# Kernel optimization log

Measured on AMD Instinct MI355X. Metric: run time of the kernel, lower is better.

The kernel has to match this reference:

```python
import jax, jax.numpy as jnp
import numpy as np

BQ, BP, L, CIN, H1, H2, COUT = 32, 256, 16, 8192, 256, 32, 8192


def _conv_block(x, w1, b1, w2, b2, w3, b3):
    # x: (B, L, H1) -> Conv1d stack over token dim with residual, as in self.convs
    h = jnp.transpose(x, (0, 2, 1))  # (B, H1, L)
    for w, b in ((w1, b1), (w2, b2), (w3, b3)):
        h = jax.lax.conv_general_dilated(h, w, (1,), [(2, 2)],
                                         dimension_numbers=('NCH', 'OIH', 'NCH'))
        h = jax.nn.relu(h + b[None, :, None])
    return jnp.transpose(h, (0, 2, 1)) + x


def setup_inputs() -> dict:
    key = jax.random.key(0)
    ks = jax.random.split(key, 16)
    query_x = (jax.random.uniform(ks[0], (BQ, L, CIN)) < 0.01).astype(jnp.float32)
    poi_x = (jax.random.uniform(ks[1], (BP, L, CIN)) < 0.01).astype(jnp.float32)
    query_loc = jax.random.uniform(ks[2], (BQ, 2)) * 100.0
    poi_loc = jax.random.uniform(ks[3], (BP, 2)) * 100.0
    enc_w = jax.random.normal(ks[4], (H1, CIN)) * 0.02
    conv_w1 = jax.random.normal(ks[5], (H1, H1, 5)) * 0.02
    conv_w2 = jax.random.normal(ks[6], (H1, H1, 5)) * 0.02
    conv_w3 = jax.random.normal(ks[7], (H1, H1, 5)) * 0.02
    conv_b1 = jnp.zeros((H1,), jnp.float32)
    conv_b2 = jnp.zeros((H1,), jnp.float32)
    conv_b3 = jnp.zeros((H1,), jnp.float32)
    dec_w1 = jax.random.normal(ks[8], (H2, 2 * H1)) * 0.05
    dec_b1 = jnp.zeros((H2,), jnp.float32)
    dec_w2 = jax.random.normal(ks[9], (H2, H2)) * 0.1
    dec_b2 = jnp.zeros((H2,), jnp.float32)
    # torch init fills this with 0; use small randn so the path is non-trivial
    dec_w3 = jax.random.normal(ks[10], (COUT, H2)) * 0.01
    a = jnp.asarray(1.0, jnp.float32)
    b = jnp.asarray(0.0, jnp.float32)
    c = jnp.asarray(1.0, jnp.float32)
    d = jnp.asarray(0.0, jnp.float32)
    return dict(query_x=query_x, query_loc=query_loc, poi_x=poi_x, poi_loc=poi_loc,
                enc_w=enc_w, conv_w1=conv_w1, conv_b1=conv_b1, conv_w2=conv_w2,
                conv_b2=conv_b2, conv_w3=conv_w3, conv_b3=conv_b3,
                dec_w1=dec_w1, dec_b1=dec_b1, dec_w2=dec_w2, dec_b2=dec_b2,
                dec_w3=dec_w3, a=a, b=b, c=c, d=d)


def reference(query_x, query_loc, poi_x, poi_loc, enc_w, conv_w1, conv_b1,
              conv_w2, conv_b2, conv_w3, conv_b3, dec_w1, dec_b1, dec_w2,
              dec_b2, dec_w3, a, b, c, d):
    # --- encode ---
    q_h = _conv_block(query_x @ enc_w.T, conv_w1, conv_b1, conv_w2, conv_b2, conv_w3, conv_b3)
    p_h = _conv_block(poi_x @ enc_w.T, conv_w1, conv_b1, conv_w2, conv_b2, conv_w3, conv_b3)
    q_emb = q_h.mean(axis=1)  # (Bq, H1)
    p_emb = p_h.mean(axis=1)  # (Bp, H1)
    # --- bloom masks ---
    q_bloom = jnp.minimum(query_x.sum(axis=1), 1.0)  # (Bq, 8192)
    p_bloom = jnp.minimum(poi_x.sum(axis=1), 1.0)    # (Bp, 8192)
    interaction = q_bloom[:, None, :] * p_bloom[None, :, :]  # (Bq, Bp, 8192)
    q_bits = q_bloom.sum(axis=-1, keepdims=True)             # (Bq, 1)
    # --- pairwise MLP decode ---
    bq, bp = q_emb.shape[0], p_emb.shape[0]
    all_embed = jnp.concatenate([
        jnp.broadcast_to(q_emb[:, None, :], (bq, bp, q_emb.shape[-1])),
        jnp.broadcast_to(p_emb[None, :, :], (bq, bp, p_emb.shape[-1])),
    ], axis=-1)  # (Bq, Bp, 2*H1)
    h = jax.nn.relu(all_embed)
    h = jax.nn.relu(h @ dec_w1.T + dec_b1)
    h = jax.nn.relu(h @ dec_w2.T + dec_b2)
    w = h @ dec_w3.T  # (Bq, Bp, 8192)
    weights = jnp.where(w >= 0, w, w * 0.125) + 1.0  # LeakyReLU(1/8) + 1
    desc_sim = (interaction * weights).sum(axis=-1) / q_bits  # (Bq, Bp)
    # --- geo-distance fusion ---
    dist = jnp.sqrt(((query_loc[:, None, :] - poi_loc[None, :, :]) ** 2).sum(axis=-1))
    mean = desc_sim.mean(axis=-1, keepdims=True)
    std = jnp.std(desc_sim, axis=-1, keepdims=True, ddof=1)  # torch.std is unbiased
    desc_sim = (desc_sim - mean) / (std + 1e-6)
    dist_sim = -jnp.log(dist + 1.0)
    return (c - jax.nn.sigmoid(a * desc_sim + b)) * (dist_sim - d)
```

## Files before the change

kernel.cpp:

```cpp
#include <hip/hip_runtime.h>

#define NB 288
#define NBQ 32
#define NBP 256
#define LTOK 16
#define CIN 8192
#define H1 256
#define H2 32
#define MASKW 256
#define XROW 264
#define IDXCAP 208

typedef __attribute__((ext_vector_type(8))) short short8;
typedef __attribute__((ext_vector_type(4))) float f32x4;

__device__ __forceinline__ unsigned short f2bf(float f) {
    unsigned u = __float_as_uint(f);
    u += 0x7fffu + ((u >> 16) & 1u);
    return (unsigned short)(u >> 16);
}

__global__ __launch_bounds__(256) void k_transpose_pack(const float* __restrict__ w,
                                                        unsigned* __restrict__ wtp) {
    __shared__ float tile[32][33];
    int k0 = blockIdx.x * 32;
    int h0 = blockIdx.y * 32;
    int tx = threadIdx.x & 31, ty = threadIdx.x >> 5;
#pragma unroll
    for (int i = 0; i < 32; i += 8)
        tile[ty + i][tx] = w[(h0 + ty + i) * CIN + k0 + tx];
    __syncthreads();
    int kl = threadIdx.x >> 3, pw = threadIdx.x & 7;
#pragma unroll
    for (int u = 0; u < 2; ++u) {
        int p = pw + u * 8;
        unsigned lo = f2bf(tile[2 * p][kl]);
        unsigned hi = f2bf(tile[2 * p + 1][kl]);
        wtp[(size_t)(k0 + kl) * 128 + (h0 >> 1) + p] = (hi << 16) | lo;
    }
}

__global__ __launch_bounds__(256) void k_wprep(const float* __restrict__ w1,
                                               const float* __restrict__ w2,
                                               const float* __restrict__ w3,
                                               unsigned short* __restrict__ wtb,
                                               unsigned* __restrict__ wtp) {
    int bx = blockIdx.x;
    if (bx == 0 && threadIdx.x < 128) wtp[(size_t)8192 * 128 + threadIdx.x] = 0;
    int l = bx / 1280;
    int r = bx - l * 1280;
    int o = r / 5;
    int d = r - o * 5;
    int i = threadIdx.x;
    const float* w = (l == 0) ? w1 : (l == 1) ? w2 : w3;
    wtb[(size_t)l * 327680 + (size_t)o * 1280 + d * 256 + i] =
        f2bf(w[(size_t)o * 1280 + i * 5 + d]);
}

__global__ __launch_bounds__(256) void k_w3pack(const float* __restrict__ w3,
                                                unsigned* __restrict__ w3p) {
    int idx = blockIdx.x * 256 + threadIdx.x;
    int k = idx >> 4, pw = idx & 15;
    unsigned lo = f2bf(w3[k * 32 + 2 * pw]);
    unsigned hi = f2bf(w3[k * 32 + 2 * pw + 1]);
    w3p[idx] = (hi << 16) | lo;
}

__global__ __launch_bounds__(256) void k_scan(const float* __restrict__ qx,
                                              const float* __restrict__ px,
                                              int* __restrict__ idxl,
                                              int* __restrict__ cnts,
                                              unsigned* __restrict__ masks) {
    int row = blockIdx.x;
    int b = row >> 4;
    const float* x = (b < NBQ) ? (qx + (size_t)row * CIN)
                               : (px + (size_t)(row - NBQ * LTOK) * CIN);
    __shared__ int cnt;
    int tid = threadIdx.x;
    if (tid == 0) cnt = 0;
    __syncthreads();
    const float4* x4 = (const float4*)x;
    float4 r[8];
#pragma unroll
    for (int j = 0; j < 8; ++j) r[j] = x4[j * 256 + tid];
    int* il = idxl + (size_t)row * IDXCAP;
#pragma unroll
    for (int j = 0; j < 8; ++j) {
        unsigned ox = __float_as_uint(r[j].x) | __float_as_uint(r[j].y) |
                      __float_as_uint(r[j].z) | __float_as_uint(r[j].w);
        if (ox) {
            int base = (j * 256 + tid) * 4;
            float vv[4] = {r[j].x, r[j].y, r[j].z, r[j].w};
#pragma unroll
            for (int c = 0; c < 4; ++c) {
                if (vv[c] != 0.f) {
                    int k = base + c;
                    int p = atomicAdd(&cnt, 1);
                    if (p < 192) il[p] = k;
                    atomicOr(&masks[b * MASKW + (k >> 5)], 1u << (k & 31));
                }
            }
        }
    }
    __syncthreads();
    int n = min(cnt, 192);
    if (tid == 0) cnts[row] = n;
    for (int i = n + tid; i < 200; i += 256) il[i] = 8192;
}

__global__ __launch_bounds__(128) void k_gather(const unsigned* __restrict__ wtp,
                                                const int* __restrict__ idxl,
                                                const int* __restrict__ cnts,
                                                float* __restrict__ encoded,
                                                unsigned* __restrict__ xbufu) {
    int row = blockIdx.x, tid = threadIdx.x;
    int n = cnts[row];
    const int* il = idxl + (size_t)row * IDXCAP;
    float aL = 0.f, aH = 0.f;
    for (int j = 0; j < n; j += 8) {
        int4 ia = *(const int4*)(il + j);
        int4 ib = *(const int4*)(il + j + 4);
        int id[8] = {ia.x, ia.y, ia.z, ia.w, ib.x, ib.y, ib.z, ib.w};
#pragma unroll
        for (int u = 0; u < 8; ++u) {
            unsigned v = wtp[(size_t)id[u] * 128 + tid];
            aL += __uint_as_float(v << 16);
            aH += __uint_as_float(v & 0xffff0000u);
        }
    }
    ((float2*)encoded)[(size_t)row * 128 + tid] = float2{aL, aH};
    unsigned bl = f2bf(aL), bh = f2bf(aH);
    xbufu[(size_t)row * 128 + tid] = (bh << 16) | bl;
}

__global__ __launch_bounds__(256) void k_cgemm(const unsigned short* __restrict__ actIn,
                                               unsigned short* __restrict__ actOut,
                                               float* __restrict__ actOutF,
                                               const unsigned short* __restrict__ wl,
                                               const float* __restrict__ bias,
                                               int last) {
    __shared__ unsigned short Als[2 * 20 * XROW];
    __shared__ unsigned short Bls[32 * XROW];
    int tid = threadIdx.x;
    int m0 = blockIdx.x * 32, n0 = blockIdx.y * 32;

    int* Ai = (int*)Als;
#pragma unroll
    for (int i = tid; i < 20 * XROW; i += 256) Ai[i] = 0;
    __syncthreads();

    int row = tid >> 3, part = tid & 7;
    {
        const short8* src = (const short8*)(actIn + (size_t)(m0 + row) * 256 + part * 32);
        unsigned short* dst = Als + ((row >> 4) * 20 + (row & 15) + 2) * XROW + part * 32;
#pragma unroll
        for (int j = 0; j < 4; ++j) *(short8*)(dst + j * 8) = src[j];
    }
    const unsigned short* bsrc = wl + (size_t)(n0 + row) * 1280 + part * 32;
    short8 rb[4];
#pragma unroll
    for (int j = 0; j < 4; ++j) rb[j] = *(const short8*)(bsrc + j * 8);

    int lane = tid & 63, wave = tid >> 6;
    int lane15 = lane & 15, quad = lane >> 4;
    int wm = wave & 1, wn = wave >> 1;
    unsigned short* bdst = Bls + row * XROW + part * 32;

    f32x4 acc = (f32x4){0.f, 0.f, 0.f, 0.f};

#pragma unroll 1
    for (int d = 0; d < 5; ++d) {
#pragma unroll
        for (int j = 0; j < 4; ++j) *(short8*)(bdst + j * 8) = rb[j];
        __syncthreads();
        if (d < 4) {
            const unsigned short* s2 = bsrc + (d + 1) * 256;
#pragma unroll
            for (int j = 0; j < 4; ++j) rb[j] = *(const short8*)(s2 + j * 8);
        }
        const unsigned short* ap = Als + (wm * 20 + lane15 + d) * XROW + quad * 8;
        const unsigned short* bp = Bls + (wn * 16 + lane15) * XROW + quad * 8;
#pragma unroll
        for (int kk = 0; kk < 8; ++kk) {
            short8 av = *(const short8*)(ap + kk * 32);
            short8 bv = *(const short8*)(bp + kk * 32);
            acc = __builtin_amdgcn_mfma_f32_16x16x32_bf16(av, bv, acc, 0, 0, 0);
        }
        __syncthreads();
    }

    int o = n0 + wn * 16 + lane15;
    float bv = bias[o];
    int rbase = m0 + wm * 16 + quad * 4;
#pragma unroll
    for (int r = 0; r < 4; ++r) {
        float v = fmaxf(acc[r] + bv, 0.f);
        if (last) actOutF[(size_t)(rbase + r) * 256 + o] = v;
        else      actOut[(size_t)(rbase + r) * 256 + o] = f2bf(v);
    }
}

__global__ __launch_bounds__(256) void k_ab(const float* __restrict__ actF,
                                            const float* __restrict__ encoded,
                                            const float* __restrict__ w1,
                                            float* __restrict__ Cmat) {
    int b = blockIdx.x, tid = threadIdx.x;
    __shared__ float e[256];
    __shared__ float red[256];
    float s = 0.f;
#pragma unroll
    for (int t = 0; t < 16; ++t)
        s += actF[((size_t)b * 16 + t) * 256 + tid] + encoded[((size_t)b * 16 + t) * 256 + tid];
    e[tid] = fmaxf(s * (1.f / 16.f), 0.f);
    __syncthreads();
    int o = tid & 31, seg = tid >> 5;
    const float* wr = w1 + (size_t)o * 512 + (b < NBQ ? 0 : 256) + seg * 32;
    float v = 0.f;
#pragma unroll
    for (int i = 0; i < 32; ++i) v = fmaf(wr[i], e[seg * 32 + i], v);
    red[tid] = v; __syncthreads();
    if (tid < 128) red[tid] += red[tid + 128]; __syncthreads();
    if (tid < 64)  red[tid] += red[tid + 64];  __syncthreads();
    if (tid < 32) {
        red[tid] += red[tid + 32];
        Cmat[b * 32 + tid] = red[tid];
    }
}

__global__ __launch_bounds__(256) void k_pair(const float* __restrict__ Cmat,
                                              const float* __restrict__ b1,
                                              const float* __restrict__ w2,
                                              const float* __restrict__ b2,
                                              const unsigned* __restrict__ w3p,
                                              const unsigned* __restrict__ masks,
                                              float* __restrict__ desc) {
    int p = blockIdx.x, q = blockIdx.y;
    __shared__ float h1[32];
    __shared__ __align__(16) float h2s[32];
    __shared__ int idxs[3072];
    __shared__ int cnt;
    __shared__ float wsum[4], wq[4];
    int tid = threadIdx.x;
    if (tid == 0) cnt = 0;
    __syncthreads();
    unsigned mq = masks[q * MASKW + tid];
    unsigned m = mq & masks[(NBQ + p) * MASKW + tid];
    int nb = __popc(m);
    if (nb) {
        int pos = atomicAdd(&cnt, nb);
        while (m) {
            int bit = __ffs(m) - 1;
            m &= m - 1;
            idxs[pos++] = tid * 32 + bit;
        }
    }
    if (tid < 32)
        h1[tid] = fmaxf(Cmat[q * 32 + tid] + Cmat[(NBQ + p) * 32 + tid] + b1[tid], 0.f);
    __syncthreads();
    if (tid < 32) {
        float s = b2[tid];
#pragma unroll
        for (int j = 0; j < 32; ++j) s = fmaf(w2[tid * 32 + j], h1[j], s);
        h2s[tid] = fmaxf(s, 0.f);
    }
    __syncthreads();
    int n = cnt;
    int rowi = tid >> 2, part = tid & 3;
    float h2v[8];
#pragma unroll
    for (int j = 0; j < 8; ++j) h2v[j] = h2s[part * 8 + j];
    float local = 0.f;
    for (int base = 0; base < n; base += 64) {
        int r = base + rowi;
        bool act = r < n;
        float dot = 0.f;
        if (act) {
            uint4 wv = *(const uint4*)(w3p + (size_t)idxs[r] * 16 + part * 4);
            unsigned wu[4] = {wv.x, wv.y, wv.z, wv.w};
#pragma unroll
            for (int u = 0; u < 4; ++u) {
                dot += __uint_as_float(wu[u] << 16) * h2v[2 * u];
                dot += __uint_as_float(wu[u] & 0xffff0000u) * h2v[2 * u + 1];
            }
        }
        dot += __shfl_xor(dot, 1);
        dot += __shfl_xor(dot, 2);
        if (act && part == 0)
            local += 1.f + (dot >= 0.f ? dot : dot * 0.125f);
    }
    float qcf = (float)__popc(mq);
#pragma unroll
    for (int st = 1; st < 64; st <<= 1) {
        local += __shfl_xor(local, st);
        qcf   += __shfl_xor(qcf, st);
    }
    if ((tid & 63) == 0) { wsum[tid >> 6] = local; wq[tid >> 6] = qcf; }
    __syncthreads();
    if (tid == 0) {
        float t  = wsum[0] + wsum[1] + wsum[2] + wsum[3];
        float qb = wq[0] + wq[1] + wq[2] + wq[3];
        desc[q * 256 + p] = t / qb;
    }
}

__global__ __launch_bounds__(256) void k_final(const float* __restrict__ desc,
                                               const float* __restrict__ qloc,
                                               const float* __restrict__ ploc,
                                               const float* __restrict__ sa,
                                               const float* __restrict__ sb,
                                               const float* __restrict__ sc,
                                               const float* __restrict__ sd,
                                               float* __restrict__ out) {
    __shared__ float red[256];
    int q = blockIdx.x, tid = threadIdx.x;
    float v = desc[q * 256 + tid];
    red[tid] = v; __syncthreads();
    for (int st = 128; st > 0; st >>= 1) {
        if (tid < st) red[tid] += red[tid + st];
        __syncthreads();
    }
    float mean = red[0] * (1.f / 256.f);
    __syncthreads();
    float dv = v - mean;
    red[tid] = dv * dv; __syncthreads();
    for (int st = 128; st > 0; st >>= 1) {
        if (tid < st) red[tid] += red[tid + st];
        __syncthreads();
    }
    float var = red[0] * (1.f / 255.f);
    float norm = dv / (sqrtf(var) + 1e-6f);
    float dx = qloc[q * 2]     - ploc[tid * 2];
    float dy = qloc[q * 2 + 1] - ploc[tid * 2 + 1];
    float dist = sqrtf(dx * dx + dy * dy);
    float z = sa[0] * norm + sb[0];
    float sig = 1.f / (1.f + expf(-z));
    out[q * 256 + tid] = (sc[0] - sig) * (-logf(dist + 1.f) - sd[0]);
}

extern "C" void kernel_launch(void* const* d_in, const int* in_sizes, int n_in,
                              void* d_out, int out_size, void* d_ws, size_t ws_size,
                              hipStream_t stream) {
    const float* qx   = (const float*)d_in[0];
    const float* qloc = (const float*)d_in[1];
    const float* px   = (const float*)d_in[2];
    const float* ploc = (const float*)d_in[3];
    const float* encw = (const float*)d_in[4];
    const float* cw1  = (const float*)d_in[5];
    const float* cb1  = (const float*)d_in[6];
    const float* cw2  = (const float*)d_in[7];
    const float* cb2  = (const float*)d_in[8];
    const float* cw3  = (const float*)d_in[9];
    const float* cb3  = (const float*)d_in[10];
    const float* dw1  = (const float*)d_in[11];
    const float* db1  = (const float*)d_in[12];
    const float* dw2  = (const float*)d_in[13];
    const float* db2  = (const float*)d_in[14];
    const float* dw3  = (const float*)d_in[15];
    const float* sa   = (const float*)d_in[16];
    const float* sb   = (const float*)d_in[17];
    const float* sc   = (const float*)d_in[18];
    const float* sd   = (const float*)d_in[19];

    char* w = (char*)d_ws;
    unsigned*       wtp     = (unsigned*)w;       w += (size_t)8193 * 128 * 4;
    float*          encoded = (float*)w;          w += (size_t)NB * LTOK * H1 * 4;
    unsigned short* xbuf    = (unsigned short*)w; w += (size_t)NB * LTOK * H1 * 2;
    unsigned short* act1    = (unsigned short*)w; w += (size_t)NB * LTOK * H1 * 2;
    unsigned short* act2    = (unsigned short*)w; w += (size_t)NB * LTOK * H1 * 2;
    float*          actF    = (float*)w;          w += (size_t)NB * LTOK * H1 * 4;
    unsigned short* wtb     = (unsigned short*)w; w += (size_t)3 * 256 * 1280 * 2;
    unsigned*       w3p     = (unsigned*)w;       w += (size_t)CIN * 16 * 4;
    int*            idxl    = (int*)w;            w += (size_t)NB * LTOK * IDXCAP * 4;
    int*            cnts    = (int*)w;            w += (size_t)NB * LTOK * 4;
    float*          Cmat    = (float*)w;          w += (size_t)NB * H2 * 4;
    unsigned*       masks   = (unsigned*)w;       w += (size_t)NB * MASKW * 4;
    float*          desc    = (float*)w;          w += (size_t)NBQ * NBP * 4;

    hipMemsetAsync(masks, 0, (size_t)NB * MASKW * 4, stream);
    k_transpose_pack<<<dim3(CIN / 32, H1 / 32), 256, 0, stream>>>(encw, wtp);
    k_wprep<<<3840, 256, 0, stream>>>(cw1, cw2, cw3, wtb, wtp);
    k_w3pack<<<512, 256, 0, stream>>>(dw3, w3p);
    k_scan<<<NB * LTOK, 256, 0, stream>>>(qx, px, idxl, cnts, masks);
    k_gather<<<NB * LTOK, 128, 0, stream>>>(wtp, idxl, cnts, encoded, (unsigned*)xbuf);
    dim3 cgrid(NB * LTOK / 32, 8);
    k_cgemm<<<cgrid, 256, 0, stream>>>(xbuf, act1, actF, wtb,              cb1, 0);
    k_cgemm<<<cgrid, 256, 0, stream>>>(act1, act2, actF, wtb + 327680,     cb2, 0);
    k_cgemm<<<cgrid, 256, 0, stream>>>(act2, act1, actF, wtb + 2 * 327680, cb3, 1);
    k_ab<<<NB, 256, 0, stream>>>(actF, encoded, dw1, Cmat);
    k_pair<<<dim3(NBP, NBQ), 256, 0, stream>>>(Cmat, db1, dw2, db2, w3p, masks, desc);
    k_final<<<NBQ, 256, 0, stream>>>(desc, qloc, ploc, sa, sb, sc, sd, (float*)d_out);
}
```

Baseline: 351.2 us.

## Fuse prep kernels, scan+gather, and conv3 with token-mean decoder projection

The three weight-prep kernels and the memset are merged into one launch. Scan and gather now run in a single kernel that keeps the index list in shared memory and atomically accumulates per-sample encoder sums, so the fp32 encoded buffer is gone. The last conv GEMM reduces its output over tokens, adds the residual sum and projects through dec_w1 with atomics into Cmat, which removes the fp32 activation write and the separate k_ab kernel. In exchange, float atomics make the summation order nondeterministic.

```diff
diff --git a/kernel.cpp b/kernel.cpp
--- a/kernel.cpp
+++ b/kernel.cpp
@@ -9,7 +9,6 @@
 #define H2 32
 #define MASKW 256
 #define XROW 264
-#define IDXCAP 208
 
 typedef __attribute__((ext_vector_type(8))) short short8;
 typedef __attribute__((ext_vector_type(4))) float f32x4;
@@ -20,62 +19,71 @@
     return (unsigned short)(u >> 16);
 }
 
-__global__ __launch_bounds__(256) void k_transpose_pack(const float* __restrict__ w,
-                                                        unsigned* __restrict__ wtp) {
-    __shared__ float tile[32][33];
-    int k0 = blockIdx.x * 32;
-    int h0 = blockIdx.y * 32;
-    int tx = threadIdx.x & 31, ty = threadIdx.x >> 5;
-#pragma unroll
-    for (int i = 0; i < 32; i += 8)
-        tile[ty + i][tx] = w[(h0 + ty + i) * CIN + k0 + tx];
-    __syncthreads();
-    int kl = threadIdx.x >> 3, pw = threadIdx.x & 7;
-#pragma unroll
-    for (int u = 0; u < 2; ++u) {
-        int p = pw + u * 8;
-        unsigned lo = f2bf(tile[2 * p][kl]);
-        unsigned hi = f2bf(tile[2 * p + 1][kl]);
-        wtp[(size_t)(k0 + kl) * 128 + (h0 >> 1) + p] = (hi << 16) | lo;
-    }
-}
-
-__global__ __launch_bounds__(256) void k_wprep(const float* __restrict__ w1,
-                                               const float* __restrict__ w2,
-                                               const float* __restrict__ w3,
-                                               unsigned short* __restrict__ wtb,
-                                               unsigned* __restrict__ wtp) {
-    int bx = blockIdx.x;
-    if (bx == 0 && threadIdx.x < 128) wtp[(size_t)8192 * 128 + threadIdx.x] = 0;
-    int l = bx / 1280;
-    int r = bx - l * 1280;
-    int o = r / 5;
-    int d = r - o * 5;
-    int i = threadIdx.x;
-    const float* w = (l == 0) ? w1 : (l == 1) ? w2 : w3;
-    wtb[(size_t)l * 327680 + (size_t)o * 1280 + d * 256 + i] =
-        f2bf(w[(size_t)o * 1280 + i * 5 + d]);
-}
-
-__global__ __launch_bounds__(256) void k_w3pack(const float* __restrict__ w3,
-                                                unsigned* __restrict__ w3p) {
-    int idx = blockIdx.x * 256 + threadIdx.x;
-    int k = idx >> 4, pw = idx & 15;
-    unsigned lo = f2bf(w3[k * 32 + 2 * pw]);
-    unsigned hi = f2bf(w3[k * 32 + 2 * pw + 1]);
-    w3p[idx] = (hi << 16) | lo;
-}
-
-__global__ __launch_bounds__(256) void k_scan(const float* __restrict__ qx,
-                                              const float* __restrict__ px,
-                                              int* __restrict__ idxl,
-                                              int* __restrict__ cnts,
-                                              unsigned* __restrict__ masks) {
+__global__ __launch_bounds__(256) void k_prep(const float* __restrict__ encw,
+                                              const float* __restrict__ w1,
+                                              const float* __restrict__ w2,
+                                              const float* __restrict__ w3c,
+                                              const float* __restrict__ dw3,
+                                              unsigned* __restrict__ wtp,
+                                              unsigned short* __restrict__ wtb,
+                                              unsigned* __restrict__ w3p,
+                                              unsigned* __restrict__ masks,
+                                              float* __restrict__ esum,
+                                              float* __restrict__ Cmat) {
+    int g = blockIdx.x, tid = threadIdx.x;
+    if (g < 2048) {
+        __shared__ float tile[32][33];
+        int k0 = (g >> 3) * 32, h0 = (g & 7) * 32;
+        int tx = tid & 31, ty = tid >> 5;
+#pragma unroll
+        for (int i = 0; i < 32; i += 8)
+            tile[ty + i][tx] = encw[(h0 + ty + i) * CIN + k0 + tx];
+        __syncthreads();
+        int kl = tid >> 3, pw = tid & 7;
+#pragma unroll
+        for (int u = 0; u < 2; ++u) {
+            int p = pw + u * 8;
+            unsigned lo = f2bf(tile[2 * p][kl]);
+            unsigned hi = f2bf(tile[2 * p + 1][kl]);
+            wtp[(size_t)(k0 + kl) * 128 + (h0 >> 1) + p] = (hi << 16) | lo;
+        }
+    } else if (g < 5888) {
+        int bx = g - 2048;
+        int l = bx / 1280;
+        int r = bx - l * 1280;
+        int o = r / 5;
+        int d = r - o * 5;
+        const float* w = (l == 0) ? w1 : (l == 1) ? w2 : w3c;
+        wtb[(size_t)l * 327680 + (size_t)o * 1280 + d * 256 + tid] =
+            f2bf(w[(size_t)o * 1280 + tid * 5 + d]);
+    } else if (g < 6400) {
+        int idx = (g - 5888) * 256 + tid;
+        int k = idx >> 4, pw = idx & 15;
+        unsigned lo = f2bf(dw3[k * 32 + 2 * pw]);
+        unsigned hi = f2bf(dw3[k * 32 + 2 * pw + 1]);
+        w3p[idx] = (hi << 16) | lo;
+    } else {
+        int b = g - 6400;
+        masks[b * MASKW + tid] = 0u;
+        esum[b * 256 + tid] = 0.f;
+        if (tid < 32) Cmat[b * 32 + tid] = 0.f;
+        if (b == 0 && tid < 128) wtp[(size_t)8192 * 128 + tid] = 0u;
+    }
+}
+
+__global__ __launch_bounds__(256) void k_scanG(const float* __restrict__ qx,
+                                               const float* __restrict__ px,
+                                               const unsigned* __restrict__ wtp,
+                                               unsigned* __restrict__ masks,
+                                               float* __restrict__ esum,
+                                               unsigned* __restrict__ xbufu) {
     int row = blockIdx.x;
     int b = row >> 4;
     const float* x = (b < NBQ) ? (qx + (size_t)row * CIN)
                                : (px + (size_t)(row - NBQ * LTOK) * CIN);
+    __shared__ int idxs[200];
     __shared__ int cnt;
+    __shared__ float sL[2][128], sH[2][128];
     int tid = threadIdx.x;
     if (tid == 0) cnt = 0;
     __syncthreads();
@@ -83,7 +91,6 @@
     float4 r[8];
 #pragma unroll
     for (int j = 0; j < 8; ++j) r[j] = x4[j * 256 + tid];
-    int* il = idxl + (size_t)row * IDXCAP;
 #pragma unroll
     for (int j = 0; j < 8; ++j) {
         unsigned ox = __float_as_uint(r[j].x) | __float_as_uint(r[j].y) |
@@ -96,7 +103,7 @@
                 if (vv[c] != 0.f) {
                     int k = base + c;
                     int p = atomicAdd(&cnt, 1);
-                    if (p < 192) il[p] = k;
+                    if (p < 192) idxs[p] = k;
                     atomicOr(&masks[b * MASKW + (k >> 5)], 1u << (k & 31));
                 }
             }
@@ -104,41 +111,36 @@
     }
     __syncthreads();
     int n = min(cnt, 192);
-    if (tid == 0) cnts[row] = n;
-    for (int i = n + tid; i < 200; i += 256) il[i] = 8192;
-}
-
-__global__ __launch_bounds__(128) void k_gather(const unsigned* __restrict__ wtp,
-                                                const int* __restrict__ idxl,
-                                                const int* __restrict__ cnts,
-                                                float* __restrict__ encoded,
-                                                unsigned* __restrict__ xbufu) {
-    int row = blockIdx.x, tid = threadIdx.x;
-    int n = cnts[row];
-    const int* il = idxl + (size_t)row * IDXCAP;
+    for (int i = n + tid; i < 200; i += 256) idxs[i] = 8192;
+    __syncthreads();
+    int pair = tid & 127, half = tid >> 7;
     float aL = 0.f, aH = 0.f;
-    for (int j = 0; j < n; j += 8) {
-        int4 ia = *(const int4*)(il + j);
-        int4 ib = *(const int4*)(il + j + 4);
-        int id[8] = {ia.x, ia.y, ia.z, ia.w, ib.x, ib.y, ib.z, ib.w};
-#pragma unroll
-        for (int u = 0; u < 8; ++u) {
-            unsigned v = wtp[(size_t)id[u] * 128 + tid];
+    for (int j0 = 0; j0 < n; j0 += 8) {
+        int4 ia = *(const int4*)(idxs + j0 + half * 4);
+        int id[4] = {ia.x, ia.y, ia.z, ia.w};
+#pragma unroll
+        for (int u = 0; u < 4; ++u) {
+            unsigned v = wtp[(size_t)id[u] * 128 + pair];
             aL += __uint_as_float(v << 16);
             aH += __uint_as_float(v & 0xffff0000u);
         }
     }
-    ((float2*)encoded)[(size_t)row * 128 + tid] = float2{aL, aH};
-    unsigned bl = f2bf(aL), bh = f2bf(aH);
-    xbufu[(size_t)row * 128 + tid] = (bh << 16) | bl;
+    sL[half][pair] = aL; sH[half][pair] = aH;
+    __syncthreads();
+    if (tid < 128) {
+        float L = sL[0][tid] + sL[1][tid];
+        float H = sH[0][tid] + sH[1][tid];
+        atomicAdd(&esum[b * 256 + 2 * tid],     L);
+        atomicAdd(&esum[b * 256 + 2 * tid + 1], H);
+        unsigned bl = f2bf(L), bh = f2bf(H);
+        xbufu[(size_t)row * 128 + tid] = (bh << 16) | bl;
+    }
 }
 
 __global__ __launch_bounds__(256) void k_cgemm(const unsigned short* __restrict__ actIn,
                                                unsigned short* __restrict__ actOut,
-                                               float* __restrict__ actOutF,
                                                const unsigned short* __restrict__ wl,
-                                               const float* __restrict__ bias,
-                                               int last) {
+                                               const float* __restrict__ bias) {
     __shared__ unsigned short Als[2 * 20 * XROW];
     __shared__ unsigned short Bls[32 * XROW];
     int tid = threadIdx.x;
@@ -167,7 +169,6 @@
     unsigned short* bdst = Bls + row * XROW + part * 32;
 
     f32x4 acc = (f32x4){0.f, 0.f, 0.f, 0.f};
-
 #pragma unroll 1
     for (int d = 0; d < 5; ++d) {
 #pragma unroll
@@ -193,37 +194,87 @@
     float bv = bias[o];
     int rbase = m0 + wm * 16 + quad * 4;
 #pragma unroll
-    for (int r = 0; r < 4; ++r) {
-        float v = fmaxf(acc[r] + bv, 0.f);
-        if (last) actOutF[(size_t)(rbase + r) * 256 + o] = v;
-        else      actOut[(size_t)(rbase + r) * 256 + o] = f2bf(v);
-    }
-}
-
-__global__ __launch_bounds__(256) void k_ab(const float* __restrict__ actF,
-                                            const float* __restrict__ encoded,
-                                            const float* __restrict__ w1,
-                                            float* __restrict__ Cmat) {
-    int b = blockIdx.x, tid = threadIdx.x;
-    __shared__ float e[256];
-    __shared__ float red[256];
-    float s = 0.f;
-#pragma unroll
-    for (int t = 0; t < 16; ++t)
-        s += actF[((size_t)b * 16 + t) * 256 + tid] + encoded[((size_t)b * 16 + t) * 256 + tid];
-    e[tid] = fmaxf(s * (1.f / 16.f), 0.f);
-    __syncthreads();
-    int o = tid & 31, seg = tid >> 5;
-    const float* wr = w1 + (size_t)o * 512 + (b < NBQ ? 0 : 256) + seg * 32;
-    float v = 0.f;
-#pragma unroll
-    for (int i = 0; i < 32; ++i) v = fmaf(wr[i], e[seg * 32 + i], v);
-    red[tid] = v; __syncthreads();
-    if (tid < 128) red[tid] += red[tid + 128]; __syncthreads();
-    if (tid < 64)  red[tid] += red[tid + 64];  __syncthreads();
-    if (tid < 32) {
-        red[tid] += red[tid + 32];
-        Cmat[b * 32 + tid] = red[tid];
+    for (int r = 0; r < 4; ++r)
+        actOut[(size_t)(rbase + r) * 256 + o] = f2bf(fmaxf(acc[r] + bv, 0.f));
+}
+
+__global__ __launch_bounds__(256) void k_cgemm3(const unsigned short* __restrict__ actIn,
+                                                const unsigned short* __restrict__ wl,
+                                                const float* __restrict__ bias,
+                                                const float* __restrict__ esum,
+                                                const float* __restrict__ dw1,
+                                                float* __restrict__ Cmat) {
+    __shared__ unsigned short Als[2 * 20 * XROW];
+    __shared__ unsigned short Bls[32 * XROW];
+    __shared__ float els[2][32];
+    int tid = threadIdx.x;
+    int m0 = blockIdx.x * 32, n0 = blockIdx.y * 32;
+
+    int* Ai = (int*)Als;
+#pragma unroll
+    for (int i = tid; i < 20 * XROW; i += 256) Ai[i] = 0;
+    __syncthreads();
+
+    int row = tid >> 3, part = tid & 7;
+    {
+        const short8* src = (const short8*)(actIn + (size_t)(m0 + row) * 256 + part * 32);
+        unsigned short* dst = Als + ((row >> 4) * 20 + (row & 15) + 2) * XROW + part * 32;
+#pragma unroll
+        for (int j = 0; j < 4; ++j) *(short8*)(dst + j * 8) = src[j];
+    }
+    const unsigned short* bsrc = wl + (size_t)(n0 + row) * 1280 + part * 32;
+    short8 rb[4];
+#pragma unroll
+    for (int j = 0; j < 4; ++j) rb[j] = *(const short8*)(bsrc + j * 8);
+
+    int lane = tid & 63, wave = tid >> 6;
+    int lane15 = lane & 15, quad = lane >> 4;
+    int wm = wave & 1, wn = wave >> 1;
+    unsigned short* bdst = Bls + row * XROW + part * 32;
+
+    f32x4 acc = (f32x4){0.f, 0.f, 0.f, 0.f};
+#pragma unroll 1
+    for (int d = 0; d < 5; ++d) {
+#pragma unroll
+        for (int j = 0; j < 4; ++j) *(short8*)(bdst + j * 8) = rb[j];
+        __syncthreads();
+        if (d < 4) {
+            const unsigned short* s2 = bsrc + (d + 1) * 256;
+#pragma unroll
+            for (int j = 0; j < 4; ++j) rb[j] = *(const short8*)(s2 + j * 8);
+        }
+        const unsigned short* ap = Als + (wm * 20 + lane15 + d) * XROW + quad * 8;
+        const unsigned short* bp = Bls + (wn * 16 + lane15) * XROW + quad * 8;
+#pragma unroll
+        for (int kk = 0; kk < 8; ++kk) {
+            short8 av = *(const short8*)(ap + kk * 32);
+            short8 bv = *(const short8*)(bp + kk * 32);
+            acc = __builtin_amdgcn_mfma_f32_16x16x32_bf16(av, bv, acc, 0, 0, 0);
+        }
+        __syncthreads();
+    }
+
+    int o_l = wn * 16 + lane15;
+    int o = n0 + o_l;
+    float bv = bias[o];
+    float sf = 0.f;
+#pragma unroll
+    for (int r = 0; r < 4; ++r) sf += fmaxf(acc[r] + bv, 0.f);
+    sf += __shfl_xor(sf, 16, 64);
+    sf += __shfl_xor(sf, 32, 64);
+    if (quad == 0) {
+        int bb = 2 * blockIdx.x + wm;
+        els[wm][o_l] = fmaxf((sf + esum[bb * 256 + o]) * (1.f / 16.f), 0.f);
+    }
+    __syncthreads();
+    if (tid < 64) {
+        int b2 = tid >> 5, op = tid & 31;
+        int bb = 2 * blockIdx.x + b2;
+        const float* wr = dw1 + (size_t)op * 512 + (bb < NBQ ? 0 : 256) + n0;
+        float s = 0.f;
+#pragma unroll
+        for (int j = 0; j < 32; ++j) s = fmaf(wr[j], els[b2][j], s);
+        atomicAdd(&Cmat[bb * 32 + op], s);
     }
 }
 
@@ -362,31 +413,24 @@
     const float* sd   = (const float*)d_in[19];
 
     char* w = (char*)d_ws;
-    unsigned*       wtp     = (unsigned*)w;       w += (size_t)8193 * 128 * 4;
-    float*          encoded = (float*)w;          w += (size_t)NB * LTOK * H1 * 4;
-    unsigned short* xbuf    = (unsigned short*)w; w += (size_t)NB * LTOK * H1 * 2;
-    unsigned short* act1    = (unsigned short*)w; w += (size_t)NB * LTOK * H1 * 2;
-    unsigned short* act2    = (unsigned short*)w; w += (size_t)NB * LTOK * H1 * 2;
-    float*          actF    = (float*)w;          w += (size_t)NB * LTOK * H1 * 4;
-    unsigned short* wtb     = (unsigned short*)w; w += (size_t)3 * 256 * 1280 * 2;
-    unsigned*       w3p     = (unsigned*)w;       w += (size_t)CIN * 16 * 4;
-    int*            idxl    = (int*)w;            w += (size_t)NB * LTOK * IDXCAP * 4;
-    int*            cnts    = (int*)w;            w += (size_t)NB * LTOK * 4;
-    float*          Cmat    = (float*)w;          w += (size_t)NB * H2 * 4;
-    unsigned*       masks   = (unsigned*)w;       w += (size_t)NB * MASKW * 4;
-    float*          desc    = (float*)w;          w += (size_t)NBQ * NBP * 4;
-
-    hipMemsetAsync(masks, 0, (size_t)NB * MASKW * 4, stream);
-    k_transpose_pack<<<dim3(CIN / 32, H1 / 32), 256, 0, stream>>>(encw, wtp);
-    k_wprep<<<3840, 256, 0, stream>>>(cw1, cw2, cw3, wtb, wtp);
-    k_w3pack<<<512, 256, 0, stream>>>(dw3, w3p);
-    k_scan<<<NB * LTOK, 256, 0, stream>>>(qx, px, idxl, cnts, masks);
-    k_gather<<<NB * LTOK, 128, 0, stream>>>(wtp, idxl, cnts, encoded, (unsigned*)xbuf);
+    unsigned*       wtp   = (unsigned*)w;       w += (size_t)8193 * 128 * 4;
+    unsigned short* xbuf  = (unsigned short*)w; w += (size_t)NB * LTOK * H1 * 2;
+    unsigned short* act1  = (unsigned short*)w; w += (size_t)NB * LTOK * H1 * 2;
+    unsigned short* act2  = (unsigned short*)w; w += (size_t)NB * LTOK * H1 * 2;
+    unsigned short* wtb   = (unsigned short*)w; w += (size_t)3 * 256 * 1280 * 2;
+    unsigned*       w3p   = (unsigned*)w;       w += (size_t)CIN * 16 * 4;
+    float*          esum  = (float*)w;          w += (size_t)NB * H1 * 4;
+    float*          Cmat  = (float*)w;          w += (size_t)NB * H2 * 4;
+    unsigned*       masks = (unsigned*)w;       w += (size_t)NB * MASKW * 4;
+    float*          desc  = (float*)w;          w += (size_t)NBQ * NBP * 4;
+
+    k_prep<<<6688, 256, 0, stream>>>(encw, cw1, cw2, cw3, dw3,
+                                     wtp, wtb, w3p, masks, esum, Cmat);
+    k_scanG<<<NB * LTOK, 256, 0, stream>>>(qx, px, wtp, masks, esum, (unsigned*)xbuf);
     dim3 cgrid(NB * LTOK / 32, 8);
-    k_cgemm<<<cgrid, 256, 0, stream>>>(xbuf, act1, actF, wtb,              cb1, 0);
-    k_cgemm<<<cgrid, 256, 0, stream>>>(act1, act2, actF, wtb + 327680,     cb2, 0);
-    k_cgemm<<<cgrid, 256, 0, stream>>>(act2, act1, actF, wtb + 2 * 327680, cb3, 1);
-    k_ab<<<NB, 256, 0, stream>>>(actF, encoded, dw1, Cmat);
+    k_cgemm<<<cgrid, 256, 0, stream>>>(xbuf, act1, wtb,          cb1);
+    k_cgemm<<<cgrid, 256, 0, stream>>>(act1, act2, wtb + 327680, cb2);
+    k_cgemm3<<<cgrid, 256, 0, stream>>>(act2, wtb + 2 * 327680, cb3, esum, dw1, Cmat);
     k_pair<<<dim3(NBP, NBQ), 256, 0, stream>>>(Cmat, db1, dw2, db2, w3p, masks, desc);
     k_final<<<NBQ, 256, 0, stream>>>(desc, qloc, ploc, sa, sb, sc, sd, (float*)d_out);
 }
```

Measured after the change: 335.6 us. 1.05x faster.
